# Kernel tuning notes

Hardware: AMD Instinct MI355X
Metric: run time of the kernel (lower is better)

## Reference

```python
import jax, jax.numpy as jnp
import numpy as np

DIM = 1024
HEADS = 16
BS = 2
N = 2048

def setup_inputs() -> dict:
    key = jax.random.key(0)
    ks = jax.random.split(key, 7)
    s = 1.0 / np.sqrt(DIM)
    seq = jax.random.normal(ks[0], (BS, N, DIM), dtype=jnp.float32)
    attn_mask = jax.random.normal(ks[1], (N, N), dtype=jnp.float32)
    Wqkv = jax.random.normal(ks[2], (DIM, 3 * DIM), dtype=jnp.float32) * s
    W1 = jax.random.normal(ks[3], (DIM, 2 * DIM), dtype=jnp.float32) * s
    b1 = jnp.zeros((2 * DIM,), dtype=jnp.float32)
    W2 = jax.random.normal(ks[4], (2 * DIM, DIM), dtype=jnp.float32) * (1.0 / np.sqrt(2 * DIM))
    b2 = jnp.zeros((DIM,), dtype=jnp.float32)
    return {"seq": seq, "attn_mask": attn_mask, "Wqkv": Wqkv,
            "W1": W1, "b1": b1, "W2": W2, "b2": b2}

def reference(seq, attn_mask, Wqkv, W1, b1, W2, b2):
    bs, n, dim = seq.shape
    h = HEADS
    hd = dim // h
    x = seq @ Wqkv                                  # [bs, n, 3*dim]
    q, k, v = jnp.split(x, 3, axis=-1)
    q = q.reshape(bs, n, h, hd)
    k = k.reshape(bs, n, h, hd)
    v = v.reshape(bs, n, h, hd)
    scores = jnp.einsum('bnhd,bmhd->bhnm', q, k) / (hd ** 0.5)
    scores = scores + attn_mask[None, None, :, :]
    attn = jax.nn.softmax(scores, axis=-1)
    out = jnp.einsum('bhnm,bmhd->bnhd', attn, v).reshape(bs, n, dim)
    # SiLU FFN (dropout inactive at inference)
    hid = jax.nn.silu(out @ W1 + b1)
    return hid @ W2 + b2
```

## Files before the change

### kernel.cpp

```cpp
#include <hip/hip_runtime.h>
#include <math.h>

#define SEQ   2048
#define NHEAD 16
#define HD    64
#define BSZ   2
#define MTOT  (BSZ*SEQ)

#define LOG2E    1.4426950408889634f
#define C_SCALE  0.18033688011112043f
#define C_MOFF  -23.083120654223414f

typedef __bf16 bf16x8 __attribute__((ext_vector_type(8)));
typedef short  s16x8  __attribute__((ext_vector_type(8)));
typedef short  s16x4  __attribute__((ext_vector_type(4)));
typedef float  f32x4  __attribute__((ext_vector_type(4)));

__device__ __forceinline__ short f2bf(float x) {
    return __builtin_bit_cast(short, (__bf16)x);
}
__device__ __forceinline__ short f2bf_bm(float x) {
    unsigned u = __builtin_bit_cast(unsigned, x);
    u = (u + 0x7fffu + ((u >> 16) & 1u)) >> 16;
    return (short)u;
}
__device__ __forceinline__ float bf2f(short h) {
    unsigned u = ((unsigned)(unsigned short)h) << 16;
    return __builtin_bit_cast(float, u);
}

__device__ __forceinline__ void gl_lds16(const short* g, short* l) {
    __builtin_amdgcn_global_load_lds(
        (const __attribute__((address_space(1))) unsigned int*)g,
        (__attribute__((address_space(3))) unsigned int*)l, 16, 0, 0);
}

__device__ __forceinline__ void tsplit_tile(const float* __restrict__ W,
    short* __restrict__ Th, short* __restrict__ Tl,
    int K, int N, int k0, int n0, float (*T)[33], int t)
{
    {
        const int kl = t >> 3;
        const int nl = (t & 7) * 4;
        const float4 v = *(const float4*)&W[(size_t)(k0 + kl) * N + n0 + nl];
        T[nl + 0][kl] = v.x; T[nl + 1][kl] = v.y;
        T[nl + 2][kl] = v.z; T[nl + 3][kl] = v.w;
    }
    __syncthreads();
    {
        const int nl = t >> 3;
        const int kl = (t & 7) * 4;
        s16x4 h, l;
        #pragma unroll
        for (int c = 0; c < 4; ++c) {
            const float x = T[nl][kl + c];
            const short hb = f2bf(x);
            h[c] = hb;
            l[c] = f2bf(x - bf2f(hb));
        }
        const size_t o = (size_t)(n0 + nl) * K + k0 + kl;
        *(s16x4*)&Th[o] = h;
        if (Tl) *(s16x4*)&Tl[o] = l;
    }
}

__global__ __launch_bounds__(256)
void prep_kernel(const float* __restrict__ seq, short* __restrict__ seqh,
                 const float* __restrict__ Wqkv, short* __restrict__ WtQh,
                 const float* __restrict__ W1, short* __restrict__ Wt1h,
                 const float* __restrict__ W2, short* __restrict__ Wt2h)
{
    __shared__ float T[32][33];
    const int t = threadIdx.x;
    const int bid = blockIdx.x;
    if (bid < 1024) {
        const size_t base = (size_t)bid * 4096 + (size_t)t * 16;
        #pragma unroll
        for (int c = 0; c < 4; ++c) {
            const float4 v = *(const float4*)&seq[base + c * 4];
            s16x4 h;
            h[0] = f2bf(v.x); h[1] = f2bf(v.y); h[2] = f2bf(v.z); h[3] = f2bf(v.w);
            *(s16x4*)&seqh[base + c * 4] = h;
        }
    } else if (bid < 4096) {
        const int idx = bid - 1024;
        tsplit_tile(Wqkv, WtQh, nullptr, 1024, 3072, (idx & 31) * 32, (idx >> 5) * 32, T, t);
    } else if (bid < 6144) {
        const int idx = bid - 4096;
        tsplit_tile(W1, Wt1h, nullptr, 1024, 2048, (idx & 31) * 32, (idx >> 5) * 32, T, t);
    } else {
        const int idx = bid - 6144;
        tsplit_tile(W2, Wt2h, nullptr, 2048, 1024, (idx & 63) * 32, (idx >> 6) * 32, T, t);
    }
}

template<int ACT, int OMODE, int VT, int NB, bool TWOB>
__global__ __launch_bounds__(256, 2)
void gemm2(const short* __restrict__ Ahg,
           const short* __restrict__ Bhg, const short* __restrict__ Blg,
           const float* __restrict__ bias,
           float* __restrict__ Cf, short* __restrict__ Chg, short* __restrict__ Clg,
           short* __restrict__ Vng,
           int M, int N, int K, int NOUT)
{
    constexpr int NJ = NB / 32;
    __shared__ short AhL[2 * 128 * 32];
    __shared__ short BhL[2 * NB * 32];
    __shared__ short BlL[TWOB ? 2 * NB * 32 : 64];

    const int t    = threadIdx.x;
    const int m0   = blockIdx.y * 128;
    const int n0   = blockIdx.x * NB;
    const int wave = t >> 6;
    const int lane = t & 63;
    const int r    = lane & 15;
    const int qd   = lane >> 4;
    const int wm   = (wave & 1) * 64;
    const int wn   = (wave >> 1) * (NB / 2);

    f32x4 acc[4][NJ];
    #pragma unroll
    for (int i = 0; i < 4; ++i)
        #pragma unroll
        for (int j = 0; j < NJ; ++j) acc[i][j] = (f32x4){0.f, 0.f, 0.f, 0.f};

    auto stage = [&](int k0, int buf) {
        const int ao = buf * 4096;
        const int bo = buf * NB * 32;
        #pragma unroll
        for (int s = 0; s < 2; ++s) {
            const int p    = wave * 2 + s;
            const int srow = p * 16 + (lane >> 2);
            const int sg   = (lane & 3) ^ ((srow >> 1) & 3);
            const size_t ga = (size_t)(m0 + srow) * K + k0 + sg * 8;
            gl_lds16(&Ahg[ga], &AhL[ao + p * 512]);
        }
        #pragma unroll
        for (int s = 0; s < NB / 64; ++s) {
            const int p    = wave * (NB / 64) + s;
            const int srow = p * 16 + (lane >> 2);
            const int sg   = (lane & 3) ^ ((srow >> 1) & 3);
            const size_t gb = (size_t)(n0 + srow) * K + k0 + sg * 8;
            gl_lds16(&Bhg[gb], &BhL[bo + p * 512]);
            if constexpr (TWOB) gl_lds16(&Blg[gb], &BlL[bo + p * 512]);
        }
    };

    stage(0, 0);

    const int NT = K / 32;
    for (int kt = 0; kt < NT; ++kt) {
        const int cur = kt & 1;
        __syncthreads();
        if (kt + 1 < NT) stage((kt + 1) * 32, 1 - cur);

        const int ao = cur * 4096;
        const int bo = cur * NB * 32;
        bf16x8 afh[4], bfh[NJ], bfl[NJ];
        #pragma unroll
        for (int i = 0; i < 4; ++i) {
            const int row = wm + i * 16 + r;
            const int oa = ao + row * 32 + ((qd ^ ((row >> 1) & 3)) * 8);
            afh[i] = __builtin_bit_cast(bf16x8, *(const s16x8*)&AhL[oa]);
        }
        #pragma unroll
        for (int j = 0; j < NJ; ++j) {
            const int row = wn + j * 16 + r;
            const int ob = bo + row * 32 + ((qd ^ ((row >> 1) & 3)) * 8);
            bfh[j] = __builtin_bit_cast(bf16x8, *(const s16x8*)&BhL[ob]);
            if constexpr (TWOB)
                bfl[j] = __builtin_bit_cast(bf16x8, *(const s16x8*)&BlL[ob]);
        }

        #pragma unroll
        for (int i = 0; i < 4; ++i)
            #pragma unroll
            for (int j = 0; j < NJ; ++j) {
                acc[i][j] = __builtin_amdgcn_mfma_f32_16x16x32_bf16(afh[i], bfh[j], acc[i][j], 0, 0, 0);
                if constexpr (TWOB)
                    acc[i][j] = __builtin_amdgcn_mfma_f32_16x16x32_bf16(afh[i], bfl[j], acc[i][j], 0, 0, 0);
            }
    }

    #pragma unroll
    for (int i = 0; i < 4; ++i)
        #pragma unroll
        for (int j = 0; j < NJ; ++j) {
            const int col = n0 + wn + j * 16 + r;
            if (VT && col >= 2048) {
                s16x4 vv;
                #pragma unroll
                for (int g = 0; g < 4; ++g) vv[g] = f2bf(acc[i][j][g]);
                const int row0 = m0 + wm + i * 16 + qd * 4;
                *(s16x4*)&Vng[(size_t)(col - 2048) * 4096 + row0] = vv;
            } else {
                const float bv = bias ? bias[col] : 0.f;
                #pragma unroll
                for (int g = 0; g < 4; ++g) {
                    const int row = m0 + wm + i * 16 + qd * 4 + g;
                    float x = acc[i][j][g] + bv;
                    if (ACT == 1) x = x / (1.0f + __expf(-x));
                    if (OMODE == 0) {
                        Cf[(size_t)row * NOUT + col] = x;
                    } else if (OMODE == 1) {
                        const short hb = f2bf(x);
                        Chg[(size_t)row * NOUT + col] = hb;
                        Clg[(size_t)row * NOUT + col] = f2bf(x - bf2f(hb));
                    } else {
                        Chg[(size_t)row * NOUT + col] = f2bf(x);
                    }
                }
            }
        }
}

__global__ __launch_bounds__(256, 2)
void attn_mfma3(const short* __restrict__ Xh, const short* __restrict__ Xl,
                const short* __restrict__ Vth, const float* __restrict__ mask,
                short* __restrict__ atth)
{
    __shared__ short KhL[2 * 64 * 64];
    __shared__ short KlL[2 * 64 * 64];
    __shared__ short VhL[2 * 64 * 64];
    __shared__ short PhL[128 * 64];

    const int t    = threadIdx.x;
    const int lane = t & 63;
    const int w    = t >> 6;
    const int r    = lane & 15;
    const int qd   = lane >> 4;
    const int b    = blockIdx.x >> 4;
    const int h    = blockIdx.x & 15;
    const int q0   = blockIdx.y * 128;

    const int srow0 = (lane >> 3);
    const int sgx   = lane & 7;

    bf16x8 qh[2][2], ql[2][2];
    #pragma unroll
    for (int i = 0; i < 2; ++i) {
        const size_t qoff = (size_t)(b * SEQ + q0 + w * 32 + i * 16 + r) * 2048 + h * 64;
        #pragma unroll
        for (int ks = 0; ks < 2; ++ks) {
            qh[i][ks] = __builtin_bit_cast(bf16x8, *(const s16x8*)&Xh[qoff + ks * 32 + qd * 8]);
            ql[i][ks] = __builtin_bit_cast(bf16x8, *(const s16x8*)&Xl[qoff + ks * 32 + qd * 8]);
        }
    }

    s16x8 ones_s;
    #pragma unroll
    for (int c = 0; c < 8; ++c) ones_s[c] = (short)0x3F80;
    const bf16x8 ones = __builtin_bit_cast(bf16x8, ones_s);

    f32x4 O[2][4], Lac[2];
    #pragma unroll
    for (int i = 0; i < 2; ++i) {
        Lac[i] = (f32x4){0.f, 0.f, 0.f, 0.f};
        #pragma unroll
        for (int j = 0; j < 4; ++j) O[i][j] = (f32x4){0.f, 0.f, 0.f, 0.f};
    }

    auto stage = [&](int kt, int buf) {
        const int k0   = kt * 64;
        const int tok0 = b * SEQ + k0;
        const int bo   = buf * 4096;
        #pragma unroll
        for (int s = 0; s < 2; ++s) {
            const int p    = w * 2 + s;
            const int srow = p * 8 + srow0;
            const int sg   = sgx ^ (srow & 7);
            const size_t gk = (size_t)(tok0 + srow) * 2048 + 1024 + h * 64 + sg * 8;
            gl_lds16(&Xh[gk], &KhL[bo + p * 512]);
            gl_lds16(&Xl[gk], &KlL[bo + p * 512]);
            const size_t gv = (size_t)(h * 64 + srow) * 4096 + (size_t)b * SEQ + k0 + sg * 8;
            gl_lds16(&Vth[gv], &VhL[bo + p * 512]);
        }
    };

    stage(0, 0);

    for (int kt = 0; kt < SEQ / 64; ++kt) {
        const int cur = kt & 1;
        const int k0  = kt * 64;

        __syncthreads();
        if (kt + 1 < SEQ / 64) stage(kt + 1, 1 - cur);

        float mreg[2][4][4];
        #pragma unroll
        for (int i = 0; i < 2; ++i)
            #pragma unroll
            for (int g = 0; g < 4; ++g) {
                const size_t mrow = (size_t)(q0 + w * 32 + i * 16 + qd * 4 + g) * SEQ + k0;
                #pragma unroll
                for (int j = 0; j < 4; ++j)
                    mreg[i][g][j] = fmaf(mask[mrow + j * 16 + r], LOG2E, C_MOFF);
            }

        const int co = cur * 4096;
        f32x4 S[2][4];
        #pragma unroll
        for (int i = 0; i < 2; ++i)
            #pragma unroll
            for (int j = 0; j < 4; ++j) S[i][j] = (f32x4){0.f, 0.f, 0.f, 0.f};
        #pragma unroll
        for (int ks = 0; ks < 2; ++ks) {
            bf16x8 kfh[4], kfl[4];
            #pragma unroll
            for (int j = 0; j < 4; ++j) {
                const int row = j * 16 + r;
                const int off = co + row * 64 + (((ks * 4 + qd) ^ (row & 7)) * 8);
                kfh[j] = __builtin_bit_cast(bf16x8, *(const s16x8*)&KhL[off]);
                kfl[j] = __builtin_bit_cast(bf16x8, *(const s16x8*)&KlL[off]);
            }
            #pragma unroll
            for (int i = 0; i < 2; ++i)
                #pragma unroll
                for (int j = 0; j < 4; ++j) {
                    S[i][j] = __builtin_amdgcn_mfma_f32_16x16x32_bf16(qh[i][ks], kfh[j], S[i][j], 0, 0, 0);
                    S[i][j] = __builtin_amdgcn_mfma_f32_16x16x32_bf16(qh[i][ks], kfl[j], S[i][j], 0, 0, 0);
                    S[i][j] = __builtin_amdgcn_mfma_f32_16x16x32_bf16(ql[i][ks], kfh[j], S[i][j], 0, 0, 0);
                }
        }

        #pragma unroll
        for (int i = 0; i < 2; ++i)
            #pragma unroll
            for (int j = 0; j < 4; ++j)
                #pragma unroll
                for (int g = 0; g < 4; ++g)
                    S[i][j][g] = exp2f(fmaf(S[i][j][g], C_SCALE, mreg[i][g][j]));

        #pragma unroll
        for (int i = 0; i < 2; ++i)
            #pragma unroll
            for (int j = 0; j < 4; ++j)
                #pragma unroll
                for (int g = 0; g < 4; ++g) {
                    const int prow = w * 32 + i * 16 + qd * 4 + g;
                    const int gr   = (j * 2 + (r >> 3)) ^ ((prow >> 1) & 7);
                    PhL[prow * 64 + gr * 8 + (r & 7)] = f2bf_bm(S[i][j][g]);
                }

        #pragma unroll
        for (int ks = 0; ks < 2; ++ks) {
            bf16x8 pfh[2], vfh[4];
            #pragma unroll
            for (int i = 0; i < 2; ++i) {
                const int row = w * 32 + i * 16 + r;
                pfh[i] = __builtin_bit_cast(bf16x8,
                    *(const s16x8*)&PhL[row * 64 + (((ks * 4 + qd) ^ ((row >> 1) & 7)) * 8)]);
            }
            #pragma unroll
            for (int j = 0; j < 4; ++j) {
                const int row = j * 16 + r;
                vfh[j] = __builtin_bit_cast(bf16x8,
                    *(const s16x8*)&VhL[co + row * 64 + (((ks * 4 + qd) ^ (row & 7)) * 8)]);
            }
            #pragma unroll
            for (int i = 0; i < 2; ++i) {
                Lac[i] = __builtin_amdgcn_mfma_f32_16x16x32_bf16(pfh[i], ones, Lac[i], 0, 0, 0);
                #pragma unroll
                for (int j = 0; j < 4; ++j)
                    O[i][j] = __builtin_amdgcn_mfma_f32_16x16x32_bf16(pfh[i], vfh[j], O[i][j], 0, 0, 0);
            }
        }
    }

    #pragma unroll
    for (int i = 0; i < 2; ++i)
        #pragma unroll
        for (int g = 0; g < 4; ++g) {
            const float inv = 1.0f / Lac[i][g];
            const size_t row = (size_t)(b * SEQ + q0 + w * 32 + i * 16 + qd * 4 + g);
            #pragma unroll
            for (int j = 0; j < 4; ++j)
                atth[row * 1024 + h * 64 + j * 16 + r] = f2bf_bm(O[i][j][g] * inv);
        }
}

extern "C" void kernel_launch(void* const* d_in, const int* in_sizes, int n_in,
                              void* d_out, int out_size, void* d_ws, size_t ws_size,
                              hipStream_t stream)
{
    const float* seq  = (const float*)d_in[0];
    const float* mask = (const float*)d_in[1];
    const float* Wqkv = (const float*)d_in[2];
    const float* W1   = (const float*)d_in[3];
    const float* b1   = (const float*)d_in[4];
    const float* W2   = (const float*)d_in[5];
    const float* b2   = (const float*)d_in[6];
    float* out = (float*)d_out;

    const size_t MiB = 1048576;
    char* B = (char*)d_ws;
    short* Xh   = (short*)(B + 0);
    short* Xl   = (short*)(B + 16 * MiB);
    short* Wt2h = (short*)(B + 32 * MiB);
    short* Wt1h = (short*)(B + 40 * MiB);
    short* WtQh = (short*)(B + 48 * MiB);
    short* hidh = (short*)(B + 0);

    short* seqh = (short*)d_out;
    short* atth = (short*)d_out;
    short* Vth  = (short*)((char*)d_out + 8 * MiB);

    prep_kernel<<<8192, 256, 0, stream>>>(seq, seqh, Wqkv, WtQh,
                                          W1, Wt1h, W2, Wt2h);

    gemm2<0, 1, 1, 128, false><<<dim3(3072 / 128, MTOT / 128), 256, 0, stream>>>(
        seqh, WtQh, nullptr, nullptr,
        nullptr, Xh, Xl, Vth, MTOT, 3072, 1024, 2048);

    attn_mfma3<<<dim3(BSZ * NHEAD, SEQ / 128), 256, 0, stream>>>(Xh, Xl, Vth, mask, atth);

    gemm2<1, 2, 0, 128, false><<<dim3(2048 / 128, MTOT / 128), 256, 0, stream>>>(
        atth, Wt1h, nullptr, b1,
        nullptr, hidh, nullptr, nullptr, MTOT, 2048, 1024, 2048);

    gemm2<0, 0, 0, 64, false><<<dim3(1024 / 64, MTOT / 128), 256, 0, stream>>>(
        hidh, Wt2h, nullptr, b2,
        out, nullptr, nullptr, nullptr, MTOT, 1024, 2048, 1024);
}
```

Before: 312.3 us.

## Widen GEMM K-tile to 64 and fold W1/W2 conversion into QKV GEMM

The GEMM kernel now stages 64-wide K tiles, with an 8-way XOR swizzle, instead of 32-wide ones. This halves the number of barrier/stage iterations and runs two MFMA sub-steps per tile, at the cost of doubled LDS use, which may lower occupancy. The unused two-B (split low part) path is removed. The W1/W2 transpose-and-convert work moves out of the prep kernel into extra blocks appended to the QKV GEMM grid, overlapping that work with the GEMM and shrinking the prep launch.

```diff
diff --git a/kernel.cpp b/kernel.cpp
--- a/kernel.cpp
+++ b/kernel.cpp
@@ -66,9 +66,7 @@
 
 __global__ __launch_bounds__(256)
 void prep_kernel(const float* __restrict__ seq, short* __restrict__ seqh,
-                 const float* __restrict__ Wqkv, short* __restrict__ WtQh,
-                 const float* __restrict__ W1, short* __restrict__ Wt1h,
-                 const float* __restrict__ W2, short* __restrict__ Wt2h)
+                 const float* __restrict__ Wqkv, short* __restrict__ WtQh)
 {
     __shared__ float T[32][33];
     const int t = threadIdx.x;
@@ -82,33 +80,45 @@
             h[0] = f2bf(v.x); h[1] = f2bf(v.y); h[2] = f2bf(v.z); h[3] = f2bf(v.w);
             *(s16x4*)&seqh[base + c * 4] = h;
         }
-    } else if (bid < 4096) {
+    } else {
         const int idx = bid - 1024;
         tsplit_tile(Wqkv, WtQh, nullptr, 1024, 3072, (idx & 31) * 32, (idx >> 5) * 32, T, t);
-    } else if (bid < 6144) {
-        const int idx = bid - 4096;
-        tsplit_tile(W1, Wt1h, nullptr, 1024, 2048, (idx & 31) * 32, (idx >> 5) * 32, T, t);
-    } else {
-        const int idx = bid - 6144;
-        tsplit_tile(W2, Wt2h, nullptr, 2048, 1024, (idx & 63) * 32, (idx >> 6) * 32, T, t);
-    }
-}
-
-template<int ACT, int OMODE, int VT, int NB, bool TWOB>
+    }
+}
+
+template<int ACT, int OMODE, int VT, int NB, int FUSE>
 __global__ __launch_bounds__(256, 2)
 void gemm2(const short* __restrict__ Ahg,
-           const short* __restrict__ Bhg, const short* __restrict__ Blg,
+           const short* __restrict__ Bhg,
            const float* __restrict__ bias,
            float* __restrict__ Cf, short* __restrict__ Chg, short* __restrict__ Clg,
            short* __restrict__ Vng,
-           int M, int N, int K, int NOUT)
+           int M, int N, int K, int NOUT,
+           const float* __restrict__ W1f, short* __restrict__ Wt1hp,
+           const float* __restrict__ W2f, short* __restrict__ Wt2hp)
 {
     constexpr int NJ = NB / 32;
-    __shared__ short AhL[2 * 128 * 32];
-    __shared__ short BhL[2 * NB * 32];
-    __shared__ short BlL[TWOB ? 2 * NB * 32 : 64];
-
-    const int t    = threadIdx.x;
+    __shared__ short AhL[2 * 128 * 64];
+    __shared__ short BhL[2 * NB * 64];
+
+    const int t = threadIdx.x;
+
+    if constexpr (FUSE) {
+        if (blockIdx.x >= (unsigned)(N / NB)) {
+            float (*T)[33] = (float(*)[33])AhL;
+            const int wid = (blockIdx.x - N / NB) * 32 + blockIdx.y;
+            if (wid < 2048) {
+                tsplit_tile(W1f, Wt1hp, nullptr, 1024, 2048,
+                            (wid & 31) * 32, (wid >> 5) * 32, T, t);
+            } else {
+                const int idx = wid - 2048;
+                tsplit_tile(W2f, Wt2hp, nullptr, 2048, 1024,
+                            (idx & 63) * 32, (idx >> 6) * 32, T, t);
+            }
+            return;
+        }
+    }
+
     const int m0   = blockIdx.y * 128;
     const int n0   = blockIdx.x * NB;
     const int wave = t >> 6;
@@ -117,6 +127,8 @@
     const int qd   = lane >> 4;
     const int wm   = (wave & 1) * 64;
     const int wn   = (wave >> 1) * (NB / 2);
+    const int lr   = lane >> 3;
+    const int lg   = lane & 7;
 
     f32x4 acc[4][NJ];
     #pragma unroll
@@ -125,61 +137,57 @@
         for (int j = 0; j < NJ; ++j) acc[i][j] = (f32x4){0.f, 0.f, 0.f, 0.f};
 
     auto stage = [&](int k0, int buf) {
-        const int ao = buf * 4096;
-        const int bo = buf * NB * 32;
-        #pragma unroll
-        for (int s = 0; s < 2; ++s) {
-            const int p    = wave * 2 + s;
-            const int srow = p * 16 + (lane >> 2);
-            const int sg   = (lane & 3) ^ ((srow >> 1) & 3);
+        const int ao = buf * 8192;
+        const int bo = buf * NB * 64;
+        #pragma unroll
+        for (int s = 0; s < 4; ++s) {
+            const int p    = wave * 4 + s;
+            const int srow = p * 8 + lr;
+            const int sg   = lg ^ (srow & 7);
             const size_t ga = (size_t)(m0 + srow) * K + k0 + sg * 8;
             gl_lds16(&Ahg[ga], &AhL[ao + p * 512]);
         }
         #pragma unroll
-        for (int s = 0; s < NB / 64; ++s) {
-            const int p    = wave * (NB / 64) + s;
-            const int srow = p * 16 + (lane >> 2);
-            const int sg   = (lane & 3) ^ ((srow >> 1) & 3);
+        for (int s = 0; s < NB / 32; ++s) {
+            const int p    = wave * (NB / 32) + s;
+            const int srow = p * 8 + lr;
+            const int sg   = lg ^ (srow & 7);
             const size_t gb = (size_t)(n0 + srow) * K + k0 + sg * 8;
             gl_lds16(&Bhg[gb], &BhL[bo + p * 512]);
-            if constexpr (TWOB) gl_lds16(&Blg[gb], &BlL[bo + p * 512]);
         }
     };
 
     stage(0, 0);
 
-    const int NT = K / 32;
+    const int NT = K / 64;
     for (int kt = 0; kt < NT; ++kt) {
         const int cur = kt & 1;
         __syncthreads();
-        if (kt + 1 < NT) stage((kt + 1) * 32, 1 - cur);
-
-        const int ao = cur * 4096;
-        const int bo = cur * NB * 32;
-        bf16x8 afh[4], bfh[NJ], bfl[NJ];
-        #pragma unroll
-        for (int i = 0; i < 4; ++i) {
-            const int row = wm + i * 16 + r;
-            const int oa = ao + row * 32 + ((qd ^ ((row >> 1) & 3)) * 8);
-            afh[i] = __builtin_bit_cast(bf16x8, *(const s16x8*)&AhL[oa]);
-        }
-        #pragma unroll
-        for (int j = 0; j < NJ; ++j) {
-            const int row = wn + j * 16 + r;
-            const int ob = bo + row * 32 + ((qd ^ ((row >> 1) & 3)) * 8);
-            bfh[j] = __builtin_bit_cast(bf16x8, *(const s16x8*)&BhL[ob]);
-            if constexpr (TWOB)
-                bfl[j] = __builtin_bit_cast(bf16x8, *(const s16x8*)&BlL[ob]);
-        }
-
-        #pragma unroll
-        for (int i = 0; i < 4; ++i)
+        if (kt + 1 < NT) stage((kt + 1) * 64, 1 - cur);
+
+        const int ao = cur * 8192;
+        const int bo = cur * NB * 64;
+        #pragma unroll
+        for (int ks = 0; ks < 2; ++ks) {
+            bf16x8 afh[4], bfh[NJ];
+            #pragma unroll
+            for (int i = 0; i < 4; ++i) {
+                const int row = wm + i * 16 + r;
+                const int oa = ao + row * 64 + (((ks * 4 + qd) ^ (row & 7)) * 8);
+                afh[i] = __builtin_bit_cast(bf16x8, *(const s16x8*)&AhL[oa]);
+            }
             #pragma unroll
             for (int j = 0; j < NJ; ++j) {
-                acc[i][j] = __builtin_amdgcn_mfma_f32_16x16x32_bf16(afh[i], bfh[j], acc[i][j], 0, 0, 0);
-                if constexpr (TWOB)
-                    acc[i][j] = __builtin_amdgcn_mfma_f32_16x16x32_bf16(afh[i], bfl[j], acc[i][j], 0, 0, 0);
-            }
+                const int row = wn + j * 16 + r;
+                const int ob = bo + row * 64 + (((ks * 4 + qd) ^ (row & 7)) * 8);
+                bfh[j] = __builtin_bit_cast(bf16x8, *(const s16x8*)&BhL[ob]);
+            }
+            #pragma unroll
+            for (int i = 0; i < 4; ++i)
+                #pragma unroll
+                for (int j = 0; j < NJ; ++j)
+                    acc[i][j] = __builtin_amdgcn_mfma_f32_16x16x32_bf16(afh[i], bfh[j], acc[i][j], 0, 0, 0);
+        }
     }
 
     #pragma unroll
@@ -405,20 +413,22 @@
     short* atth = (short*)d_out;
     short* Vth  = (short*)((char*)d_out + 8 * MiB);
 
-    prep_kernel<<<8192, 256, 0, stream>>>(seq, seqh, Wqkv, WtQh,
-                                          W1, Wt1h, W2, Wt2h);
-
-    gemm2<0, 1, 1, 128, false><<<dim3(3072 / 128, MTOT / 128), 256, 0, stream>>>(
-        seqh, WtQh, nullptr, nullptr,
-        nullptr, Xh, Xl, Vth, MTOT, 3072, 1024, 2048);
+    prep_kernel<<<4096, 256, 0, stream>>>(seq, seqh, Wqkv, WtQh);
+
+    gemm2<0, 1, 1, 128, 1><<<dim3(3072 / 128 + 128, MTOT / 128), 256, 0, stream>>>(
+        seqh, WtQh, nullptr,
+        nullptr, Xh, Xl, Vth, MTOT, 3072, 1024, 2048,
+        W1, Wt1h, W2, Wt2h);
 
     attn_mfma3<<<dim3(BSZ * NHEAD, SEQ / 128), 256, 0, stream>>>(Xh, Xl, Vth, mask, atth);
 
-    gemm2<1, 2, 0, 128, false><<<dim3(2048 / 128, MTOT / 128), 256, 0, stream>>>(
-        atth, Wt1h, nullptr, b1,
-        nullptr, hidh, nullptr, nullptr, MTOT, 2048, 1024, 2048);
-
-    gemm2<0, 0, 0, 64, false><<<dim3(1024 / 64, MTOT / 128), 256, 0, stream>>>(
-        hidh, Wt2h, nullptr, b2,
-        out, nullptr, nullptr, nullptr, MTOT, 1024, 2048, 1024);
-}
+    gemm2<1, 2, 0, 128, 0><<<dim3(2048 / 128, MTOT / 128), 256, 0, stream>>>(
+        atth, Wt1h, b1,
+        nullptr, hidh, nullptr, nullptr, MTOT, 2048, 1024, 2048,
+        nullptr, nullptr, nullptr, nullptr);
+
+    gemm2<0, 0, 0, 64, 0><<<dim3(1024 / 64, MTOT / 128), 256, 0, stream>>>(
+        hidh, Wt2h, b2,
+        out, nullptr, nullptr, nullptr, MTOT, 1024, 2048, 1024,
+        nullptr, nullptr, nullptr, nullptr);
+}
```

New measurement: 314.8 us. Within noise of the previous version (+0.8%).
